# Kernel optimization log

Hardware: AMD Instinct MI355X
Metric: run time of the kernel (lower is better)

## Reference

```python
import jax, jax.numpy as jnp
import numpy as np

N, L, S, H, D = 2, 4096, 4096, 8, 32


def setup_inputs() -> dict:
    key = jax.random.key(0)
    kq, kk, kv = jax.random.split(key, 3)
    queries = jax.random.normal(kq, (N, L, H, D), dtype=jnp.float32)
    keys = jax.random.normal(kk, (N, S, H, D), dtype=jnp.float32)
    values = jax.random.normal(kv, (N, S, H, D), dtype=jnp.float32)
    q_mask = jnp.ones((N, L), dtype=bool)
    kv_mask = jnp.ones((N, S), dtype=bool)
    return {"queries": queries, "keys": keys, "values": values,
            "q_mask": q_mask, "kv_mask": kv_mask}


def reference(queries, keys, values, q_mask, kv_mask):
    d_k = queries.shape[-1]
    scale = 1.0 / (d_k ** 0.5)
    # [N, L, S, H] logits, matching the torch einsum layout
    attn_logits = jnp.einsum('nlhd,nshd->nlsh', queries, keys) * scale
    if kv_mask is not None:
        qm = q_mask[:, :, None, None] if q_mask is not None else True
        km = kv_mask[:, None, :, None]
        mask = jnp.logical_and(qm, km)
        attn_logits = jnp.where(mask, attn_logits, -jnp.inf)
    attn_weights = jax.nn.softmax(attn_logits, axis=2)
    output = jnp.einsum('nlsh,nshd->nlhd', attn_weights, values)
    return output
```

## Files before the change

### kernel.cpp

```cpp
#include <hip/hip_runtime.h>
#include <hip/hip_bf16.h>


#define L_Q 4096
#define S_K 4096
#define H_N 8
#define D_H 32
#define SC2 0.2550565358f

typedef unsigned short u16;

using bf16x8 = __attribute__((ext_vector_type(8))) __bf16;
using f32x16 = __attribute__((ext_vector_type(16))) float;

__device__ inline u16 f2bf_bits(float x) {
  __bf16 b = (__bf16)x;
  return __builtin_bit_cast(u16, b);
}

__global__ __launch_bounds__(256) void prep_kernel(const float* __restrict__ K,
                                                   const float* __restrict__ V,
                                                   u16* __restrict__ Kb,
                                                   u16* __restrict__ Vt) {
  __shared__ __align__(16) u16 t[32][72];
  int bid = blockIdx.x;
  if (bid < 1024) {
    int tid = bid * 256 + threadIdx.x;
    int o = tid * 8;
    int d0 = o & 31;
    int row = o >> 5;
    int s = row & 4095;
    int nh = row >> 12;
    int h = nh & 7, n = nh >> 3;
    const float* src = K + (((n * S_K + s) * H_N + h) * D_H + d0);
    float4 a = *(const float4*)src;
    float4 b = *(const float4*)(src + 4);
    union { u16 us[8]; uint4 q; } r;
    r.us[0] = f2bf_bits(a.x); r.us[1] = f2bf_bits(a.y);
    r.us[2] = f2bf_bits(a.z); r.us[3] = f2bf_bits(a.w);
    r.us[4] = f2bf_bits(b.x); r.us[5] = f2bf_bits(b.y);
    r.us[6] = f2bf_bits(b.z); r.us[7] = f2bf_bits(b.w);
    *(uint4*)(Kb + o) = r.q;
  } else {
    int vb = bid - 1024;
    int nh = vb >> 6;
    int s0 = (vb & 63) * 64;
    int n = nh >> 3, h = nh & 7;
    int tidx = threadIdx.x;
    int sl = tidx >> 2;
    int d0 = (tidx & 3) * 8;
    int c = (sl & 32) | (sl & 0x13) | ((sl & 4) << 1) | ((sl & 8) >> 1);
    const float* src = V + (((n * S_K + s0 + sl) * H_N + h) * D_H + d0);
    float4 a = *(const float4*)src;
    float4 b = *(const float4*)(src + 4);
    t[d0 + 0][c] = f2bf_bits(a.x); t[d0 + 1][c] = f2bf_bits(a.y);
    t[d0 + 2][c] = f2bf_bits(a.z); t[d0 + 3][c] = f2bf_bits(a.w);
    t[d0 + 4][c] = f2bf_bits(b.x); t[d0 + 5][c] = f2bf_bits(b.y);
    t[d0 + 6][c] = f2bf_bits(b.z); t[d0 + 7][c] = f2bf_bits(b.w);
    __syncthreads();
    int d = tidx >> 3;
    int si = (tidx & 7) * 8;
    uint4 w = *(const uint4*)&t[d][si];
    int tile = (s0 >> 5) + (si >> 5);
    *(uint4*)(Vt + (nh * 131072 + tile * 1024 + d * 32 + (si & 31))) = w;
  }
}

__global__ __launch_bounds__(512) void attn_kernel(const float* __restrict__ Q,
                                                   const u16* __restrict__ Kb,
                                                   const u16* __restrict__ Vt,
                                                   float* __restrict__ Out) {
  __shared__ float comb[7][17][64];
  int bid = blockIdx.x;
  int x = bid & 7, j = bid >> 3;
  int nh = (x << 1) | (j >> 6);
  int qblk = j & 63;
  int n = nh >> 3, h = nh & 7;
  int lane = threadIdx.x & 63;
  int wid = threadIdx.x >> 6;
  int l31 = lane & 31;
  int gh = lane >> 5;
  int g8 = gh * 8;

  int qra = qblk * 64 + l31;
  int qrb = qra + 32;

  bf16x8 qf0, qf1, qf2, qf3;
  {
    const float* qp = Q + (((n * L_Q + qra) * H_N + h) * D_H);
#pragma unroll
    for (int i = 0; i < 8; i++) {
      qf0[i] = (__bf16)(qp[g8 + i] * SC2);
      qf1[i] = (__bf16)(qp[16 + g8 + i] * SC2);
    }
    qp += 32 * H_N * D_H;
#pragma unroll
    for (int i = 0; i < 8; i++) {
      qf2[i] = (__bf16)(qp[g8 + i] * SC2);
      qf3[i] = (__bf16)(qp[16 + g8 + i] * SC2);
    }
  }

  const u16* Kh = Kb + nh * (S_K * D_H);
  const u16* Vh = Vt + nh * (S_K * D_H);
  int koff = l31 * 32 + g8;

  f32x16 acc_a, acc_b, z16;
#pragma unroll
  for (int i = 0; i < 16; i++) { acc_a[i] = 0.f; acc_b[i] = 0.f; z16[i] = 0.f; }
  float lsum_a = 0.f, lsum_b = 0.f;

  bf16x8 ka0, ka1, va0, va1;

  auto group = [&](bf16x8 qx0, bf16x8 qx1, f32x16& acc, float& lsum) {
    f32x16 sv = __builtin_amdgcn_mfma_f32_32x32x16_bf16(ka0, qx0, z16, 0, 0, 0);
    sv = __builtin_amdgcn_mfma_f32_32x32x16_bf16(ka1, qx1, sv, 0, 0, 0);
    {
      float p0 = __builtin_amdgcn_exp2f(sv[0]);
      float p1 = __builtin_amdgcn_exp2f(sv[1]);
      float p2 = __builtin_amdgcn_exp2f(sv[2]);
      float p3 = __builtin_amdgcn_exp2f(sv[3]);
      float p4 = __builtin_amdgcn_exp2f(sv[4]);
      float p5 = __builtin_amdgcn_exp2f(sv[5]);
      float p6 = __builtin_amdgcn_exp2f(sv[6]);
      float p7 = __builtin_amdgcn_exp2f(sv[7]);
      lsum += ((p0 + p1) + (p2 + p3)) + ((p4 + p5) + (p6 + p7));
      bf16x8 A;
      A[0] = (__bf16)p0; A[1] = (__bf16)p1; A[2] = (__bf16)p2; A[3] = (__bf16)p3;
      A[4] = (__bf16)p4; A[5] = (__bf16)p5; A[6] = (__bf16)p6; A[7] = (__bf16)p7;
      acc = __builtin_amdgcn_mfma_f32_32x32x16_bf16(va0, A, acc, 0, 0, 0);
    }
    {
      float p0 = __builtin_amdgcn_exp2f(sv[8]);
      float p1 = __builtin_amdgcn_exp2f(sv[9]);
      float p2 = __builtin_amdgcn_exp2f(sv[10]);
      float p3 = __builtin_amdgcn_exp2f(sv[11]);
      float p4 = __builtin_amdgcn_exp2f(sv[12]);
      float p5 = __builtin_amdgcn_exp2f(sv[13]);
      float p6 = __builtin_amdgcn_exp2f(sv[14]);
      float p7 = __builtin_amdgcn_exp2f(sv[15]);
      lsum += ((p0 + p1) + (p2 + p3)) + ((p4 + p5) + (p6 + p7));
      bf16x8 A;
      A[0] = (__bf16)p0; A[1] = (__bf16)p1; A[2] = (__bf16)p2; A[3] = (__bf16)p3;
      A[4] = (__bf16)p4; A[5] = (__bf16)p5; A[6] = (__bf16)p6; A[7] = (__bf16)p7;
      acc = __builtin_amdgcn_mfma_f32_32x32x16_bf16(va1, A, acc, 0, 0, 0);
    }
  };

#define LOADK(r0, r1, t) { const u16* p_ = Kh + ((t) * 1024 + koff); \
    r0 = *(const bf16x8*)p_; r1 = *(const bf16x8*)(p_ + 16); }
#define LOADV(r0, r1, t) { const u16* p_ = Vh + ((t) * 1024 + koff); \
    r0 = *(const bf16x8*)p_; r1 = *(const bf16x8*)(p_ + 16); }

  int t0 = wid * 16;
  for (int t = t0; t < t0 + 16; t++) {
    LOADK(ka0, ka1, t);
    LOADV(va0, va1, t);
    group(qf0, qf1, acc_a, lsum_a);
    __builtin_amdgcn_sched_barrier(0);
    group(qf2, qf3, acc_b, lsum_b);
  }

  if (wid != 0) {
#pragma unroll
    for (int r = 0; r < 16; r++) comb[wid - 1][r][lane] = acc_a[r];
    comb[wid - 1][16][lane] = lsum_a;
  }
  __syncthreads();
  if (wid == 0) {
#pragma unroll
    for (int w = 0; w < 7; w++) {
#pragma unroll
      for (int r = 0; r < 16; r++) acc_a[r] += comb[w][r][lane];
      lsum_a += comb[w][16][lane];
    }
  }
  __syncthreads();
  if (wid != 0) {
#pragma unroll
    for (int r = 0; r < 16; r++) comb[wid - 1][r][lane] = acc_b[r];
    comb[wid - 1][16][lane] = lsum_b;
  }
  __syncthreads();
  if (wid == 0) {
#pragma unroll
    for (int w = 0; w < 7; w++) {
#pragma unroll
      for (int r = 0; r < 16; r++) acc_b[r] += comb[w][r][lane];
      lsum_b += comb[w][16][lane];
    }
    float inv_a = 1.0f / (lsum_a + __shfl_xor(lsum_a, 32, 64));
    float inv_b = 1.0f / (lsum_b + __shfl_xor(lsum_b, 32, 64));
    float* opa = Out + (((n * L_Q + qra) * H_N + h) * D_H) + 4 * gh;
    float* opb = Out + (((n * L_Q + qrb) * H_N + h) * D_H) + 4 * gh;
#pragma unroll
    for (int jj = 0; jj < 4; jj++) {
      float4 wa, wb;
      wa.x = acc_a[4 * jj] * inv_a;     wa.y = acc_a[4 * jj + 1] * inv_a;
      wa.z = acc_a[4 * jj + 2] * inv_a; wa.w = acc_a[4 * jj + 3] * inv_a;
      wb.x = acc_b[4 * jj] * inv_b;     wb.y = acc_b[4 * jj + 1] * inv_b;
      wb.z = acc_b[4 * jj + 2] * inv_b; wb.w = acc_b[4 * jj + 3] * inv_b;
      *(float4*)(opa + 8 * jj) = wa;
      *(float4*)(opb + 8 * jj) = wb;
    }
  }
}

extern "C" void kernel_launch(void* const* d_in, const int* in_sizes, int n_in,
                              void* d_out, int out_size, void* d_ws, size_t ws_size,
                              hipStream_t stream) {
  const float* Q = (const float*)d_in[0];
  const float* K = (const float*)d_in[1];
  const float* V = (const float*)d_in[2];
  float* Out = (float*)d_out;
  u16* Kb = (u16*)d_ws;
  u16* Vt = Kb + 2 * H_N * S_K * D_H;

  prep_kernel<<<2048, 256, 0, stream>>>(K, V, Kb, Vt);
  attn_kernel<<<1024, 512, 0, stream>>>(Q, Kb, Vt, Out);
}
```

Baseline: 68.64 us.

## Use six waves per block with double-buffered K/V prefetch and interleaved MFMAs

Cuts the attention block from 8 to 6 waves, splitting the 128 key tiles unevenly (21 or 22 per wave) and adding a min-waves-per-EU hint to the launch bounds. The inner loop now prefetches the next tile's K and V fragments into a second register set while computing the current one. It also issues both QK MFMA chains for the two query halves before the exp/PV work, giving more independent MFMA work to hide latency. The extra prefetch registers raise register pressure, and fewer waves per block means less parallelism within each block.

```diff
diff --git a/kernel.cpp b/kernel.cpp
--- a/kernel.cpp
+++ b/kernel.cpp
@@ -66,11 +66,11 @@
   }
 }
 
-__global__ __launch_bounds__(512) void attn_kernel(const float* __restrict__ Q,
-                                                   const u16* __restrict__ Kb,
-                                                   const u16* __restrict__ Vt,
-                                                   float* __restrict__ Out) {
-  __shared__ float comb[7][17][64];
+__global__ __launch_bounds__(384, 4) void attn_kernel(const float* __restrict__ Q,
+                                                      const u16* __restrict__ Kb,
+                                                      const u16* __restrict__ Vt,
+                                                      float* __restrict__ Out) {
+  __shared__ float comb[5][17][64];
   int bid = blockIdx.x;
   int x = bid & 7, j = bid >> 3;
   int nh = (x << 1) | (j >> 6);
@@ -110,11 +110,9 @@
   for (int i = 0; i < 16; i++) { acc_a[i] = 0.f; acc_b[i] = 0.f; z16[i] = 0.f; }
   float lsum_a = 0.f, lsum_b = 0.f;
 
-  bf16x8 ka0, ka1, va0, va1;
-
-  auto group = [&](bf16x8 qx0, bf16x8 qx1, f32x16& acc, float& lsum) {
-    f32x16 sv = __builtin_amdgcn_mfma_f32_32x32x16_bf16(ka0, qx0, z16, 0, 0, 0);
-    sv = __builtin_amdgcn_mfma_f32_32x32x16_bf16(ka1, qx1, sv, 0, 0, 0);
+  bf16x8 ka0, ka1, kb0, kb1, va0, va1, vb0, vb1;
+
+  auto finish = [&](f32x16 sv, bf16x8 vf0, bf16x8 vf1, f32x16& acc, float& lsum) {
     {
       float p0 = __builtin_amdgcn_exp2f(sv[0]);
       float p1 = __builtin_amdgcn_exp2f(sv[1]);
@@ -128,7 +126,7 @@
       bf16x8 A;
       A[0] = (__bf16)p0; A[1] = (__bf16)p1; A[2] = (__bf16)p2; A[3] = (__bf16)p3;
       A[4] = (__bf16)p4; A[5] = (__bf16)p5; A[6] = (__bf16)p6; A[7] = (__bf16)p7;
-      acc = __builtin_amdgcn_mfma_f32_32x32x16_bf16(va0, A, acc, 0, 0, 0);
+      acc = __builtin_amdgcn_mfma_f32_32x32x16_bf16(vf0, A, acc, 0, 0, 0);
     }
     {
       float p0 = __builtin_amdgcn_exp2f(sv[8]);
@@ -143,8 +141,17 @@
       bf16x8 A;
       A[0] = (__bf16)p0; A[1] = (__bf16)p1; A[2] = (__bf16)p2; A[3] = (__bf16)p3;
       A[4] = (__bf16)p4; A[5] = (__bf16)p5; A[6] = (__bf16)p6; A[7] = (__bf16)p7;
-      acc = __builtin_amdgcn_mfma_f32_32x32x16_bf16(va1, A, acc, 0, 0, 0);
-    }
+      acc = __builtin_amdgcn_mfma_f32_32x32x16_bf16(vf1, A, acc, 0, 0, 0);
+    }
+  };
+
+  auto tile = [&](bf16x8 kf0, bf16x8 kf1, bf16x8 vf0, bf16x8 vf1) {
+    f32x16 sva = __builtin_amdgcn_mfma_f32_32x32x16_bf16(kf0, qf0, z16, 0, 0, 0);
+    sva = __builtin_amdgcn_mfma_f32_32x32x16_bf16(kf1, qf1, sva, 0, 0, 0);
+    f32x16 svb = __builtin_amdgcn_mfma_f32_32x32x16_bf16(kf0, qf2, z16, 0, 0, 0);
+    svb = __builtin_amdgcn_mfma_f32_32x32x16_bf16(kf1, qf3, svb, 0, 0, 0);
+    finish(sva, vf0, vf1, acc_a, lsum_a);
+    finish(svb, vf0, vf1, acc_b, lsum_b);
   };
 
 #define LOADK(r0, r1, t) { const u16* p_ = Kh + ((t) * 1024 + koff); \
@@ -152,14 +159,20 @@
 #define LOADV(r0, r1, t) { const u16* p_ = Vh + ((t) * 1024 + koff); \
     r0 = *(const bf16x8*)p_; r1 = *(const bf16x8*)(p_ + 16); }
 
-  int t0 = wid * 16;
-  for (int t = t0; t < t0 + 16; t++) {
-    LOADK(ka0, ka1, t);
-    LOADV(va0, va1, t);
-    group(qf0, qf1, acc_a, lsum_a);
-    __builtin_amdgcn_sched_barrier(0);
-    group(qf2, qf3, acc_b, lsum_b);
-  }
+  int ex = wid - 1; ex = ex < 0 ? 0 : (ex > 2 ? 2 : ex);
+  int tb = wid * 21 + ex;
+  int te = tb + 21 + ((wid == 1 || wid == 2) ? 1 : 0);
+
+  LOADK(ka0, ka1, tb); LOADV(va0, va1, tb);
+  int t = tb;
+  while (t + 1 < te) {
+    LOADK(kb0, kb1, t + 1); LOADV(vb0, vb1, t + 1);
+    tile(ka0, ka1, va0, va1);
+    if (t + 2 < te) { LOADK(ka0, ka1, t + 2); LOADV(va0, va1, t + 2); }
+    tile(kb0, kb1, vb0, vb1);
+    t += 2;
+  }
+  if (t < te) tile(ka0, ka1, va0, va1);
 
   if (wid != 0) {
 #pragma unroll
@@ -169,7 +182,7 @@
   __syncthreads();
   if (wid == 0) {
 #pragma unroll
-    for (int w = 0; w < 7; w++) {
+    for (int w = 0; w < 5; w++) {
 #pragma unroll
       for (int r = 0; r < 16; r++) acc_a[r] += comb[w][r][lane];
       lsum_a += comb[w][16][lane];
@@ -184,7 +197,7 @@
   __syncthreads();
   if (wid == 0) {
 #pragma unroll
-    for (int w = 0; w < 7; w++) {
+    for (int w = 0; w < 5; w++) {
 #pragma unroll
       for (int r = 0; r < 16; r++) acc_b[r] += comb[w][r][lane];
       lsum_b += comb[w][16][lane];
@@ -217,5 +230,5 @@
   u16* Vt = Kb + 2 * H_N * S_K * D_H;
 
   prep_kernel<<<2048, 256, 0, stream>>>(K, V, Kb, Vt);
-  attn_kernel<<<1024, 512, 0, stream>>>(Q, Kb, Vt, Out);
-}
+  attn_kernel<<<1024, 384, 0, stream>>>(Q, Kb, Vt, Out);
+}
```

Result: slower. 89.76 us (+30.8%).
